# Optimization experiments

Measured on AMD Instinct MI355X. Metric: run time of the kernel, lower is better.

The kernel has to match this reference:

```python
import jax, jax.numpy as jnp
import numpy as np

N, D_IN, D_ATTN = 8192, 48, 8


def setup_inputs() -> dict:
    key = jax.random.key(0)
    ks = jax.random.split(key, 9)
    s = 1.0 / np.sqrt(D_IN)
    return {
        "x": jax.random.normal(ks[0], (N, D_IN), jnp.float32),
        "Kw": jax.random.normal(ks[1], (D_IN, D_ATTN), jnp.float32) * s,
        "Kb": jax.random.normal(ks[2], (D_ATTN,), jnp.float32) * s,
        "Qw": jax.random.normal(ks[3], (D_IN, D_ATTN), jnp.float32) * s,
        "Qb": jax.random.normal(ks[4], (D_ATTN,), jnp.float32) * s,
        "Vw": jax.random.normal(ks[5], (D_IN, D_ATTN), jnp.float32) * s,
        "Vb": jax.random.normal(ks[6], (D_ATTN,), jnp.float32) * s,
        "Zw": jax.random.normal(ks[7], (D_ATTN, D_IN), jnp.float32) * (1.0 / np.sqrt(D_ATTN)),
        "Zb": jax.random.normal(ks[8], (D_IN,), jnp.float32) * (1.0 / np.sqrt(D_ATTN)),
    }


def reference(x, Kw, Kb, Qw, Qb, Vw, Vb, Zw, Zb):
    # Tiny QKV projections: [N,48] -> [N,8]
    Xk = x @ Kw + Kb
    Xq = x @ Qw + Qb
    Xv = x @ Vw + Vb
    # Attention over the batch/row dimension: [N,8]@[8,N] -> [N,N]
    scale = jnp.sqrt(jnp.asarray(D_ATTN, jnp.float32))
    AM = jax.nn.softmax(Xk @ Xq.T / scale, axis=1)  # torch F.softmax 2D default dim=1
    Z = AM @ Xv                                      # [N,8]
    return x + (Z @ Zw + Zb)                         # residual + output proj [N,48]
```

## Files before the change

### kernel.cpp

```cpp
#include <hip/hip_runtime.h>
#include <hip/hip_fp16.h>


#define QV_OFF   32768
#define BMAX_OFF 98304
#define PART_OFF 98560

typedef _Float16 hv2 __attribute__((ext_vector_type(2)));
union HVU { unsigned u; hv2 v; };

static __device__ __forceinline__ unsigned pku(float a, float b) {
    auto t = __builtin_amdgcn_cvt_pkrtz(a, b);
    union { decltype(t) x; unsigned u; } c; c.x = t; return c.u;
}
static __device__ __forceinline__ hv2 asV(unsigned u) { HVU t; t.u = u; return t.v; }
static __device__ __forceinline__ unsigned dupL(unsigned u) {
    const unsigned lo = u & 0xFFFFu; return lo | (lo << 16);
}
static __device__ __forceinline__ unsigned dupH(unsigned u) {
    const unsigned hi = u >> 16; return hi | (hi << 16);
}
static __device__ __forceinline__ void pkfma(unsigned& d, unsigned a, unsigned b) {
    asm("v_pk_fma_f16 %0, %1, %2, %0" : "+v"(d) : "v"(a), "v"(b));
}

__global__ __launch_bounds__(256) void proj_kernel(
    const float* __restrict__ x,
    const float* __restrict__ Kw, const float* __restrict__ Kb,
    const float* __restrict__ Qw, const float* __restrict__ Qb,
    const float* __restrict__ Vw, const float* __restrict__ Vb,
    unsigned* __restrict__ Xksf16, unsigned* __restrict__ QV,
    float* __restrict__ bmax)
{
    __shared__ float xs[32 * 49];
    __shared__ float wAll[3 * 388];
    __shared__ float bs[24];
    __shared__ float outv[32][25];
    const int tid = threadIdx.x;
    const int r0 = blockIdx.x * 32;

    for (int i = tid; i < 1536; i += 256) {
        int r = i / 48, c = i - r * 48;
        xs[r * 49 + c] = x[r0 * 48 + i];
    }
    for (int i = tid; i < 384; i += 256) {
        wAll[i]       = Kw[i];
        wAll[388 + i] = Qw[i];
        wAll[776 + i] = Vw[i];
    }
    if (tid < 8)       bs[tid] = Kb[tid];
    else if (tid < 16) bs[tid] = Qb[tid - 8];
    else if (tid < 24) bs[tid] = Vb[tid - 16];
    __syncthreads();

    const int rl = tid >> 3;
    const int g  = tid & 7;
    const int c0 = 3 * g;
    const float* xr = &xs[rl * 49];
    const float* w0 = &wAll[((c0 + 0) >> 3) * 388 + ((c0 + 0) & 7)];
    const float* w1 = &wAll[((c0 + 1) >> 3) * 388 + ((c0 + 1) & 7)];
    const float* w2 = &wAll[((c0 + 2) >> 3) * 388 + ((c0 + 2) & 7)];
    float a0 = bs[c0], a1 = bs[c0 + 1], a2 = bs[c0 + 2];
    #pragma unroll
    for (int k = 0; k < 48; k++) {
        const float xv = xr[k];
        a0 = fmaf(xv, w0[k * 8], a0);
        a1 = fmaf(xv, w1[k * 8], a1);
        a2 = fmaf(xv, w2[k * 8], a2);
    }
    outv[rl][c0] = a0; outv[rl][c0 + 1] = a1; outv[rl][c0 + 2] = a2;
    __syncthreads();

    {
        const int p = tid >> 4;
        const int c = (tid >> 1) & 7;
        const int m = tid & 1;
        const int col = (m ? 16 : 8) + c;
        QV[(blockIdx.x * 16 + p) * 16 + m * 8 + c] =
            pku(outv[2 * p][col], outv[2 * p + 1][col]);
    }
    const float kscale = 0.51008732149f;
    if (tid < 32) {
        uint4 o;
        o.x = pku(outv[tid][0] * kscale, outv[tid][1] * kscale);
        o.y = pku(outv[tid][2] * kscale, outv[tid][3] * kscale);
        o.z = pku(outv[tid][4] * kscale, outv[tid][5] * kscale);
        o.w = pku(outv[tid][6] * kscale, outv[tid][7] * kscale);
        ((uint4*)Xksf16)[r0 + tid] = o;
    }
    if (tid >= 192 && tid < 224) {
        const int r = tid - 192;
        float n2 = 0.f;
        #pragma unroll
        for (int c = 0; c < 8; c++) n2 = fmaf(outv[r][8 + c], outv[r][8 + c], n2);
        #pragma unroll
        for (int off = 16; off > 0; off >>= 1)
            n2 = fmaxf(n2, __shfl_xor(n2, off, 64));
        if (r == 0) bmax[blockIdx.x] = n2;
    }
}

__global__ __launch_bounds__(64) void attn_kernel(
    const unsigned* __restrict__ Xksf16, const unsigned* __restrict__ QV,
    const float* __restrict__ bmax,
    __half* __restrict__ partH, int P)
{
    __shared__ uint4 tile4[128];
    const int lane  = threadIdx.x;
    const int g     = blockIdx.x & 31;
    const int chunk = blockIdx.x >> 5;

    float m = fmaxf(fmaxf(bmax[lane], bmax[64 + lane]),
                    fmaxf(bmax[128 + lane], bmax[192 + lane]));
    #pragma unroll
    for (int off = 32; off > 0; off >>= 1)
        m = fmaxf(m, __shfl_xor(m, off, 64));
    const float qmax2 = m;

    unsigned kd[4][8], sinit2[4], l2[4], acc[4][8];
    #pragma unroll
    for (int k = 0; k < 4; k++) {
        const int row = g * 256 + k * 64 + lane;
        const uint4 kv = ((const uint4*)Xksf16)[row];
        kd[k][0] = dupL(kv.x); kd[k][1] = dupH(kv.x);
        kd[k][2] = dupL(kv.y); kd[k][3] = dupH(kv.y);
        kd[k][4] = dupL(kv.z); kd[k][5] = dupH(kv.z);
        kd[k][6] = dupL(kv.w); kd[k][7] = dupH(kv.w);
        float kn2 = 0.f;
        #pragma unroll
        for (int c = 0; c < 8; c++) {
            const float kf = (float)asV(kd[k][c]).x;
            kn2 = fmaf(kf, kf, kn2);
        }
        const float sinit = -sqrtf(kn2 * qmax2);
        sinit2[k] = pku(sinit, sinit);
        l2[k] = 0u;
        #pragma unroll
        for (int c = 0; c < 8; c++) acc[k][c] = 0u;
    }
    const unsigned one2 = 0x3C003C00u;

    for (int t0 = 0; t0 < P; t0 += 32) {
        __syncthreads();
        tile4[lane]      = ((const uint4*)QV)[((size_t)chunk * P + t0) * 4 + lane];
        tile4[lane + 64] = ((const uint4*)QV)[((size_t)chunk * P + t0) * 4 + lane + 64];
        __syncthreads();

        #pragma unroll 2
        for (int p = 0; p < 32; p++) {
            const uint4 qp0 = tile4[p * 4 + 0];
            const uint4 qp1 = tile4[p * 4 + 1];
            const uint4 vp0 = tile4[p * 4 + 2];
            const uint4 vp1 = tile4[p * 4 + 3];
            #pragma unroll
            for (int k = 0; k < 4; k++) {
                unsigned s2 = sinit2[k];
                pkfma(s2, kd[k][0], qp0.x);
                pkfma(s2, kd[k][1], qp0.y);
                pkfma(s2, kd[k][2], qp0.z);
                pkfma(s2, kd[k][3], qp0.w);
                pkfma(s2, kd[k][4], qp1.x);
                pkfma(s2, kd[k][5], qp1.y);
                pkfma(s2, kd[k][6], qp1.z);
                pkfma(s2, kd[k][7], qp1.w);
                const hv2 sv = asV(s2);
                const float pa = __builtin_amdgcn_exp2f((float)sv.x);
                const float pb = __builtin_amdgcn_exp2f((float)sv.y);
                const unsigned ph = pku(pa, pb);
                pkfma(l2[k], ph, one2);
                pkfma(acc[k][0], ph, vp0.x);
                pkfma(acc[k][1], ph, vp0.y);
                pkfma(acc[k][2], ph, vp0.z);
                pkfma(acc[k][3], ph, vp0.w);
                pkfma(acc[k][4], ph, vp1.x);
                pkfma(acc[k][5], ph, vp1.y);
                pkfma(acc[k][6], ph, vp1.z);
                pkfma(acc[k][7], ph, vp1.w);
            }
        }
    }

    #pragma unroll
    for (int k = 0; k < 4; k++) {
        const int row = g * 256 + k * 64 + lane;
        #pragma unroll
        for (int c = 0; c < 8; c++) {
            const hv2 a = asV(acc[k][c]);
            partH[((size_t)(chunk * 9 + c) << 13) + row] =
                __float2half_rn((float)a.x + (float)a.y);
        }
        const hv2 lv = asV(l2[k]);
        partH[((size_t)(chunk * 9 + 8) << 13) + row] =
            __float2half_rn((float)lv.x + (float)lv.y);
    }
}

__global__ __launch_bounds__(256) void finish_kernel(
    const float* __restrict__ x,
    const float* __restrict__ Zw, const float* __restrict__ Zb,
    const __half* __restrict__ partH, float* __restrict__ out, int nch)
{
    __shared__ float red[4][64][10];
    __shared__ float Zs[64][9];
    __shared__ float zw_s[384];
    __shared__ float zb_s[48];
    const int tid = threadIdx.x;
    const int r0 = blockIdx.x * 64;

    for (int i = tid; i < 384; i += 256) zw_s[i] = Zw[i];
    if (tid < 48) zb_s[tid] = Zb[tid];

    const int r = tid & 63, s = tid >> 6;
    const int row = r0 + r;
    const int cps = nch >> 2;
    float a[9];
    #pragma unroll
    for (int c = 0; c < 9; c++) a[c] = 0.f;
    for (int i = 0; i < cps; i++) {
        const int ch = s * cps + i;
        const __half* p = partH + ((size_t)(ch * 9) << 13) + row;
        #pragma unroll
        for (int c = 0; c < 9; c++) a[c] += __half2float(p[(size_t)c << 13]);
    }
    #pragma unroll
    for (int c = 0; c < 9; c++) red[s][r][c] = a[c];
    __syncthreads();
    if (tid < 64) {
        float b[9];
        #pragma unroll
        for (int c = 0; c < 9; c++)
            b[c] = red[0][tid][c] + red[1][tid][c] + red[2][tid][c] + red[3][tid][c];
        const float inv = 1.0f / b[8];
        #pragma unroll
        for (int c = 0; c < 8; c++) Zs[tid][c] = b[c] * inv;
    }
    __syncthreads();

    for (int e = tid; e < 64 * 48; e += 256) {
        const int rr = e / 48, c = e - rr * 48;
        float o = x[r0 * 48 + e] + zb_s[c];
        #pragma unroll
        for (int k = 0; k < 8; k++) o = fmaf(Zs[rr][k], zw_s[k * 48 + c], o);
        out[r0 * 48 + e] = o;
    }
}

extern "C" void kernel_launch(void* const* d_in, const int* in_sizes, int n_in,
                              void* d_out, int out_size, void* d_ws, size_t ws_size,
                              hipStream_t stream) {
    const float* x  = (const float*)d_in[0];
    const float* Kw = (const float*)d_in[1];
    const float* Kb = (const float*)d_in[2];
    const float* Qw = (const float*)d_in[3];
    const float* Qb = (const float*)d_in[4];
    const float* Vw = (const float*)d_in[5];
    const float* Vb = (const float*)d_in[6];
    const float* Zw = (const float*)d_in[7];
    const float* Zb = (const float*)d_in[8];
    float* out = (float*)d_out;

    float* ws = (float*)d_ws;
    unsigned* Xksf16 = (unsigned*)ws;
    unsigned* QV     = (unsigned*)(ws + QV_OFF);
    float* bmax      = ws + BMAX_OFF;
    __half* partH    = (__half*)(ws + PART_OFF);

    int nch = 128;
    while (nch > 4 &&
           (size_t)PART_OFF * 4 + (size_t)nch * 9 * 8192 * 2 > ws_size) nch >>= 1;
    const int P = 4096 / nch;

    proj_kernel<<<256, 256, 0, stream>>>(x, Kw, Kb, Qw, Qb, Vw, Vb,
                                         Xksf16, QV, bmax);
    attn_kernel<<<32 * nch, 64, 0, stream>>>(Xksf16, QV, bmax, partH, P);
    finish_kernel<<<128, 256, 0, stream>>>(x, Zw, Zb, partH, out, nch);
}
```

Measured before the change: 128.1 us.

## Switch attention inner loop from packed fp16 FMA to fp32 math

Keys are now stored in fp32 and the attention inner loop computes scores, exponentials and accumulations in scalar fp32 rather than packed fp16 pairs. Q/V are stored per row instead of interleaved row pairs. The attention blocks grow to 256 threads, and each block loads its whole Q/V chunk into shared memory once instead of looping over tiles. The aim is better accuracy and less per-iteration conversion and packing overhead. In exchange it loses the two-rows-per-instruction throughput of packed fp16 and needs more registers per thread.

```diff
diff --git a/kernel.cpp b/kernel.cpp
--- a/kernel.cpp
+++ b/kernel.cpp
@@ -2,9 +2,9 @@
 #include <hip/hip_fp16.h>
 
 
-#define QV_OFF   32768
-#define BMAX_OFF 98304
-#define PART_OFF 98560
+#define QV_OFF   65536
+#define BMAX_OFF 131072
+#define PART_OFF 131328
 
 typedef _Float16 hv2 __attribute__((ext_vector_type(2)));
 union HVU { unsigned u; hv2 v; };
@@ -14,22 +14,13 @@
     union { decltype(t) x; unsigned u; } c; c.x = t; return c.u;
 }
 static __device__ __forceinline__ hv2 asV(unsigned u) { HVU t; t.u = u; return t.v; }
-static __device__ __forceinline__ unsigned dupL(unsigned u) {
-    const unsigned lo = u & 0xFFFFu; return lo | (lo << 16);
-}
-static __device__ __forceinline__ unsigned dupH(unsigned u) {
-    const unsigned hi = u >> 16; return hi | (hi << 16);
-}
-static __device__ __forceinline__ void pkfma(unsigned& d, unsigned a, unsigned b) {
-    asm("v_pk_fma_f16 %0, %1, %2, %0" : "+v"(d) : "v"(a), "v"(b));
-}
 
 __global__ __launch_bounds__(256) void proj_kernel(
     const float* __restrict__ x,
     const float* __restrict__ Kw, const float* __restrict__ Kb,
     const float* __restrict__ Qw, const float* __restrict__ Qb,
     const float* __restrict__ Vw, const float* __restrict__ Vb,
-    unsigned* __restrict__ Xksf16, unsigned* __restrict__ QV,
+    float* __restrict__ Xksf32, unsigned* __restrict__ QV,
     float* __restrict__ bmax)
 {
     __shared__ float xs[32 * 49];
@@ -71,22 +62,15 @@
     outv[rl][c0] = a0; outv[rl][c0 + 1] = a1; outv[rl][c0 + 2] = a2;
     __syncthreads();
 
+    const float kscale = 0.51008732149f;
     {
-        const int p = tid >> 4;
-        const int c = (tid >> 1) & 7;
-        const int m = tid & 1;
-        const int col = (m ? 16 : 8) + c;
-        QV[(blockIdx.x * 16 + p) * 16 + m * 8 + c] =
-            pku(outv[2 * p][col], outv[2 * p + 1][col]);
-    }
-    const float kscale = 0.51008732149f;
-    if (tid < 32) {
-        uint4 o;
-        o.x = pku(outv[tid][0] * kscale, outv[tid][1] * kscale);
-        o.y = pku(outv[tid][2] * kscale, outv[tid][3] * kscale);
-        o.z = pku(outv[tid][4] * kscale, outv[tid][5] * kscale);
-        o.w = pku(outv[tid][6] * kscale, outv[tid][7] * kscale);
-        ((uint4*)Xksf16)[r0 + tid] = o;
+        const int r = tid >> 3, c = tid & 7;
+        Xksf32[(r0 + r) * 8 + c] = outv[r][c] * kscale;
+    }
+    {
+        const int j = tid >> 3, d = tid & 7;
+        const int base = (d < 4) ? (8 + 2 * d) : (16 + 2 * (d - 4));
+        QV[(r0 + j) * 8 + d] = pku(outv[j][base], outv[j][base + 1]);
     }
     if (tid >= 192 && tid < 224) {
         const int r = tid - 192;
@@ -100,15 +84,20 @@
     }
 }
 
-__global__ __launch_bounds__(64) void attn_kernel(
-    const unsigned* __restrict__ Xksf16, const unsigned* __restrict__ QV,
+__global__ __launch_bounds__(256) void attn_kernel(
+    const float* __restrict__ Xksf32, const unsigned* __restrict__ QV,
     const float* __restrict__ bmax,
-    __half* __restrict__ partH, int P)
+    __half* __restrict__ partH, int C)
 {
-    __shared__ uint4 tile4[128];
-    const int lane  = threadIdx.x;
-    const int g     = blockIdx.x & 31;
-    const int chunk = blockIdx.x >> 5;
+    __shared__ uint4 tile4[256];
+    const int tid  = threadIdx.x;
+    const int lane = tid & 63;
+    const int wv   = tid >> 6;
+    const int g    = blockIdx.x & 7;
+    const int ch   = blockIdx.x >> 3;
+
+    for (int i = tid; i < C * 2; i += 256)
+        tile4[i] = ((const uint4*)QV)[(size_t)ch * C * 2 + i];
 
     float m = fmaxf(fmaxf(bmax[lane], bmax[64 + lane]),
                     fmaxf(bmax[128 + lane], bmax[192 + lane]));
@@ -117,81 +106,66 @@
         m = fmaxf(m, __shfl_xor(m, off, 64));
     const float qmax2 = m;
 
-    unsigned kd[4][8], sinit2[4], l2[4], acc[4][8];
+    const int rbase = g * 1024 + wv * 256 + lane;
+    float kf[4][8], sinit[4], l[4], acc[4][8];
+    const float4* Xk4 = (const float4*)Xksf32;
     #pragma unroll
     for (int k = 0; k < 4; k++) {
-        const int row = g * 256 + k * 64 + lane;
-        const uint4 kv = ((const uint4*)Xksf16)[row];
-        kd[k][0] = dupL(kv.x); kd[k][1] = dupH(kv.x);
-        kd[k][2] = dupL(kv.y); kd[k][3] = dupH(kv.y);
-        kd[k][4] = dupL(kv.z); kd[k][5] = dupH(kv.z);
-        kd[k][6] = dupL(kv.w); kd[k][7] = dupH(kv.w);
+        const int row = rbase + 64 * k;
+        const float4 ka = Xk4[row * 2], kb = Xk4[row * 2 + 1];
+        kf[k][0] = ka.x; kf[k][1] = ka.y; kf[k][2] = ka.z; kf[k][3] = ka.w;
+        kf[k][4] = kb.x; kf[k][5] = kb.y; kf[k][6] = kb.z; kf[k][7] = kb.w;
         float kn2 = 0.f;
         #pragma unroll
-        for (int c = 0; c < 8; c++) {
-            const float kf = (float)asV(kd[k][c]).x;
-            kn2 = fmaf(kf, kf, kn2);
+        for (int c = 0; c < 8; c++) kn2 = fmaf(kf[k][c], kf[k][c], kn2);
+        sinit[k] = -sqrtf(kn2 * qmax2);
+        l[k] = 0.f;
+        #pragma unroll
+        for (int c = 0; c < 8; c++) acc[k][c] = 0.f;
+    }
+
+    __syncthreads();
+
+    #pragma unroll 2
+    for (int j = 0; j < C; j++) {
+        const uint4 qd = tile4[j * 2];
+        const uint4 vd = tile4[j * 2 + 1];
+        float qf[8], vf[8];
+        { hv2 h = asV(qd.x); qf[0] = (float)h.x; qf[1] = (float)h.y; }
+        { hv2 h = asV(qd.y); qf[2] = (float)h.x; qf[3] = (float)h.y; }
+        { hv2 h = asV(qd.z); qf[4] = (float)h.x; qf[5] = (float)h.y; }
+        { hv2 h = asV(qd.w); qf[6] = (float)h.x; qf[7] = (float)h.y; }
+        { hv2 h = asV(vd.x); vf[0] = (float)h.x; vf[1] = (float)h.y; }
+        { hv2 h = asV(vd.y); vf[2] = (float)h.x; vf[3] = (float)h.y; }
+        { hv2 h = asV(vd.z); vf[4] = (float)h.x; vf[5] = (float)h.y; }
+        { hv2 h = asV(vd.w); vf[6] = (float)h.x; vf[7] = (float)h.y; }
+        #pragma unroll
+        for (int k = 0; k < 4; k++) {
+            float s = sinit[k];
+            s = fmaf(kf[k][0], qf[0], s); s = fmaf(kf[k][1], qf[1], s);
+            s = fmaf(kf[k][2], qf[2], s); s = fmaf(kf[k][3], qf[3], s);
+            s = fmaf(kf[k][4], qf[4], s); s = fmaf(kf[k][5], qf[5], s);
+            s = fmaf(kf[k][6], qf[6], s); s = fmaf(kf[k][7], qf[7], s);
+            const float p = __builtin_amdgcn_exp2f(s);
+            l[k] += p;
+            acc[k][0] = fmaf(p, vf[0], acc[k][0]);
+            acc[k][1] = fmaf(p, vf[1], acc[k][1]);
+            acc[k][2] = fmaf(p, vf[2], acc[k][2]);
+            acc[k][3] = fmaf(p, vf[3], acc[k][3]);
+            acc[k][4] = fmaf(p, vf[4], acc[k][4]);
+            acc[k][5] = fmaf(p, vf[5], acc[k][5]);
+            acc[k][6] = fmaf(p, vf[6], acc[k][6]);
+            acc[k][7] = fmaf(p, vf[7], acc[k][7]);
         }
-        const float sinit = -sqrtf(kn2 * qmax2);
-        sinit2[k] = pku(sinit, sinit);
-        l2[k] = 0u;
-        #pragma unroll
-        for (int c = 0; c < 8; c++) acc[k][c] = 0u;
-    }
-    const unsigned one2 = 0x3C003C00u;
-
-    for (int t0 = 0; t0 < P; t0 += 32) {
-        __syncthreads();
-        tile4[lane]      = ((const uint4*)QV)[((size_t)chunk * P + t0) * 4 + lane];
-        tile4[lane + 64] = ((const uint4*)QV)[((size_t)chunk * P + t0) * 4 + lane + 64];
-        __syncthreads();
-
-        #pragma unroll 2
-        for (int p = 0; p < 32; p++) {
-            const uint4 qp0 = tile4[p * 4 + 0];
-            const uint4 qp1 = tile4[p * 4 + 1];
-            const uint4 vp0 = tile4[p * 4 + 2];
-            const uint4 vp1 = tile4[p * 4 + 3];
-            #pragma unroll
-            for (int k = 0; k < 4; k++) {
-                unsigned s2 = sinit2[k];
-                pkfma(s2, kd[k][0], qp0.x);
-                pkfma(s2, kd[k][1], qp0.y);
-                pkfma(s2, kd[k][2], qp0.z);
-                pkfma(s2, kd[k][3], qp0.w);
-                pkfma(s2, kd[k][4], qp1.x);
-                pkfma(s2, kd[k][5], qp1.y);
-                pkfma(s2, kd[k][6], qp1.z);
-                pkfma(s2, kd[k][7], qp1.w);
-                const hv2 sv = asV(s2);
-                const float pa = __builtin_amdgcn_exp2f((float)sv.x);
-                const float pb = __builtin_amdgcn_exp2f((float)sv.y);
-                const unsigned ph = pku(pa, pb);
-                pkfma(l2[k], ph, one2);
-                pkfma(acc[k][0], ph, vp0.x);
-                pkfma(acc[k][1], ph, vp0.y);
-                pkfma(acc[k][2], ph, vp0.z);
-                pkfma(acc[k][3], ph, vp0.w);
-                pkfma(acc[k][4], ph, vp1.x);
-                pkfma(acc[k][5], ph, vp1.y);
-                pkfma(acc[k][6], ph, vp1.z);
-                pkfma(acc[k][7], ph, vp1.w);
-            }
-        }
     }
 
     #pragma unroll
     for (int k = 0; k < 4; k++) {
-        const int row = g * 256 + k * 64 + lane;
-        #pragma unroll
-        for (int c = 0; c < 8; c++) {
-            const hv2 a = asV(acc[k][c]);
-            partH[((size_t)(chunk * 9 + c) << 13) + row] =
-                __float2half_rn((float)a.x + (float)a.y);
-        }
-        const hv2 lv = asV(l2[k]);
-        partH[((size_t)(chunk * 9 + 8) << 13) + row] =
-            __float2half_rn((float)lv.x + (float)lv.y);
+        const int row = rbase + 64 * k;
+        #pragma unroll
+        for (int c = 0; c < 8; c++)
+            partH[((size_t)(ch * 9 + c) << 13) + row] = __float2half_rn(acc[k][c]);
+        partH[((size_t)(ch * 9 + 8) << 13) + row] = __float2half_rn(l[k]);
     }
 }
 
@@ -260,18 +234,18 @@
     float* out = (float*)d_out;
 
     float* ws = (float*)d_ws;
-    unsigned* Xksf16 = (unsigned*)ws;
-    unsigned* QV     = (unsigned*)(ws + QV_OFF);
-    float* bmax      = ws + BMAX_OFF;
-    __half* partH    = (__half*)(ws + PART_OFF);
+    float* Xksf32 = ws;
+    unsigned* QV  = (unsigned*)(ws + QV_OFF);
+    float* bmax   = ws + BMAX_OFF;
+    __half* partH = (__half*)(ws + PART_OFF);
 
     int nch = 128;
-    while (nch > 4 &&
+    while (nch > 64 &&
            (size_t)PART_OFF * 4 + (size_t)nch * 9 * 8192 * 2 > ws_size) nch >>= 1;
-    const int P = 4096 / nch;
+    const int C = 8192 / nch;
 
     proj_kernel<<<256, 256, 0, stream>>>(x, Kw, Kb, Qw, Qb, Vw, Vb,
-                                         Xksf16, QV, bmax);
-    attn_kernel<<<32 * nch, 64, 0, stream>>>(Xksf16, QV, bmax, partH, P);
+                                         Xksf32, QV, bmax);
+    attn_kernel<<<8 * nch, 256, 0, stream>>>(Xksf32, QV, bmax, partH, C);
     finish_kernel<<<128, 256, 0, stream>>>(x, Zw, Zb, partH, out, nch);
 }
```

New measurement: 136.3 us. 6.5% more time.
